# Kernel tuning notes

Measured on AMD Instinct MI355X. Metric: run time of the kernel, lower is better.

## Reference

```python
import jax, jax.numpy as jnp
import numpy as np

SCENE_BOUND = 1.5

# SH degree-2 constants (standard real spherical harmonics, Plenoxels convention)
C0 = 0.28209479177387814
C1 = 0.4886025119029199
C2_0 = 1.0925484305920792
C2_1 = -1.0925484305920792
C2_2 = 0.31539156525252005
C2_3 = -1.0925484305920792
C2_4 = 0.5462742152960396


def sh_basis(dirs):
    # dirs: (N,3) unit vectors -> (N,9) deg-2 SH basis
    x, y, z = dirs[:, 0], dirs[:, 1], dirs[:, 2]
    xx, yy, zz = x * x, y * y, z * z
    return jnp.stack([
        jnp.full_like(x, C0),
        -C1 * y,
        C1 * z,
        -C1 * x,
        C2_0 * x * y,
        C2_1 * y * z,
        C2_2 * (2.0 * zz - xx - yy),
        C2_3 * x * z,
        C2_4 * (xx - yy),
    ], axis=-1)


def grid_sample_trilinear(vol, pts):
    """torch F.grid_sample(mode=bilinear, padding=zeros, align_corners=True).

    vol: (C, D, H, W); pts: (N, 3) in [-1, 1], ordered (x, y, z) where
    x indexes W, y indexes H, z indexes D (torch convention).
    Returns (N, C).
    """
    C, D, H, W = vol.shape
    # align_corners=True: -1 -> 0, +1 -> size-1
    fx = (pts[:, 0] + 1.0) * 0.5 * (W - 1)
    fy = (pts[:, 1] + 1.0) * 0.5 * (H - 1)
    fz = (pts[:, 2] + 1.0) * 0.5 * (D - 1)
    x0 = jnp.floor(fx); y0 = jnp.floor(fy); z0 = jnp.floor(fz)
    wx1 = fx - x0; wy1 = fy - y0; wz1 = fz - z0
    x0i = x0.astype(jnp.int32); y0i = y0.astype(jnp.int32); z0i = z0.astype(jnp.int32)

    out = jnp.zeros((pts.shape[0], C), dtype=vol.dtype)
    for dz in (0, 1):
        zi = z0i + dz
        wz = wz1 if dz == 1 else (1.0 - wz1)
        for dy in (0, 1):
            yi = y0i + dy
            wy = wy1 if dy == 1 else (1.0 - wy1)
            for dx in (0, 1):
                xi = x0i + dx
                wx = wx1 if dx == 1 else (1.0 - wx1)
                inb = ((xi >= 0) & (xi < W) & (yi >= 0) & (yi < H)
                       & (zi >= 0) & (zi < D))
                xc = jnp.clip(xi, 0, W - 1)
                yc = jnp.clip(yi, 0, H - 1)
                zc = jnp.clip(zi, 0, D - 1)
                val = vol[:, zc, yc, xc]  # (C, N) gather
                w = (wx * wy * wz) * inb.astype(vol.dtype)
                out = out + val.T * w[:, None]
    return out


def setup_inputs() -> dict:
    key = jax.random.key(0)
    k1, k2, k3 = jax.random.split(key, 3)
    N, R, C = 2_000_000, 128, 28
    xyz = (jax.random.uniform(k1, (N, 3), jnp.float32) * 2.0 - 1.0) * SCENE_BOUND
    vd = jax.random.normal(k2, (N, 3), jnp.float32)
    view_dirs = vd / jnp.linalg.norm(vd, axis=-1, keepdims=True)
    density_grid = jnp.full((1, 1, R, R, R), 0.1, jnp.float32)
    sh_grid = jax.random.normal(k3, (1, C - 1, R, R, R), jnp.float32) * 0.01
    return {"xyz": xyz, "view_dirs": view_dirs,
            "density_grid": density_grid, "sh_grid": sh_grid}


def reference(xyz, view_dirs, density_grid, sh_grid):
    # combined grid (1, C, R, R, R) -> (C, D, H, W)
    vol = jnp.concatenate([density_grid, sh_grid], axis=1)[0]
    # query: trilinear interp at normalized coords
    feats = grid_sample_trilinear(vol, xyz / SCENE_BOUND)  # (N, C)
    # decode
    density = jax.nn.relu(feats[:, 0])  # (N,)
    sh_coef = feats[:, 1:].reshape(feats.shape[0], 3, 9)  # (N, 3, 9)
    basis = sh_basis(view_dirs)  # (N, 9)
    rgb = jax.nn.sigmoid(jnp.einsum('ncb,nb->nc', sh_coef, basis))  # (N, 3)
    return density, rgb
```

## Files before the change

### kernel.cpp

```cpp
#include <hip/hip_runtime.h>
#include <hip/hip_fp16.h>
#include <math.h>

#define GR 128
#define NCH 28


__device__ __forceinline__ float sigmoidf_(float x) {
    return 1.0f / (1.0f + expf(-x));
}

__device__ __forceinline__ __half2 u2h2(unsigned int u) {
    return *reinterpret_cast<__half2*>(&u);
}

__global__ __launch_bounds__(256) void pack_kernel(
    const float* __restrict__ dens,
    const float* __restrict__ sh,
    uint4* __restrict__ vol,
    int V)
{
    int t = blockIdx.x * blockDim.x + threadIdx.x;
    int v0 = t * 2;
    if (v0 >= V) return;

    float2 dd = *reinterpret_cast<const float2*>(dens + v0);
    float sa[27], sb[27];
#pragma unroll
    for (int q = 0; q < 27; ++q) {
        float2 s2 = *reinterpret_cast<const float2*>(sh + (size_t)q * (size_t)V + v0);
        sa[q] = s2.x;
        sb[q] = s2.y;
    }

#pragma unroll
    for (int j = 0; j < 2; ++j) {
        const float* sv = (j == 0) ? sa : sb;
        float dv = (j == 0) ? dd.x : dd.y;

        float mp = 0.0f, mn = 0.0f;
#pragma unroll
        for (int q = 0; q < 27; ++q) {
            float x = sv[q];
            mp = fmaxf(mp, x);
            mn = fmaxf(mn, -x);
        }
        float tq = fmaxf(fmaxf(mp * (1.0f / 7.0f), mn * 0.125f), 7.5e-9f);
        int ex = (int)((__float_as_uint(tq) >> 23) & 0xFFu) - 126;
        int e = min(max(ex + 14, 0), 15);
        float invf = __uint_as_float((unsigned int)(141 - e) << 23);

        unsigned int w[4];
#pragma unroll
        for (int d = 0; d < 3; ++d) {
            unsigned int acc = 0;
#pragma unroll
            for (int b = 0; b < 8; ++b) {
                int n = (int)rintf(sv[8 * d + b] * invf) + 8;
                n = min(max(n, 0), 15);
                acc |= (unsigned int)n << (4 * b);
            }
            w[d] = acc;
        }
        int n24 = min(max((int)rintf(sv[24] * invf) + 8, 0), 15);
        int n25 = min(max((int)rintf(sv[25] * invf) + 8, 0), 15);
        int n26 = min(max((int)rintf(sv[26] * invf) + 8, 0), 15);
        unsigned int dh = (unsigned int)__half_as_ushort(__float2half_rn(dv));
        w[3] = (unsigned int)n24 | ((unsigned int)n25 << 4) | ((unsigned int)n26 << 8)
             | ((unsigned int)e << 12) | (dh << 16);

        vol[v0 + j] = make_uint4(w[0], w[1], w[2], w[3]);
    }
}

__global__ __launch_bounds__(256) void sample_kernel(
    const float* __restrict__ xyz,
    const float* __restrict__ vdirs,
    const uint4* __restrict__ vol,
    float* __restrict__ out,
    int N)
{
    int i = blockIdx.x * blockDim.x + threadIdx.x;
    if (i >= N) return;

    const float kk = (1.0f / 1.5f) * 0.5f * (float)(GR - 1);
    const float cc = 0.5f * (float)(GR - 1);
    float fx = fminf(fmaxf(fmaf(xyz[3*i+0], kk, cc), 0.0f), (float)(GR - 1));
    float fy = fminf(fmaxf(fmaf(xyz[3*i+1], kk, cc), 0.0f), (float)(GR - 1));
    float fz = fminf(fmaxf(fmaf(xyz[3*i+2], kk, cc), 0.0f), (float)(GR - 1));

    int x0 = (int)fx, y0 = (int)fy, z0 = (int)fz;
    float wx1 = fx - (float)x0, wy1 = fy - (float)y0, wz1 = fz - (float)z0;
    float wx0 = 1.0f - wx1, wy0 = 1.0f - wy1, wz0 = 1.0f - wz1;
    int x1 = min(x0 + 1, GR - 1);
    int y1 = min(y0 + 1, GR - 1);
    int z1 = min(z0 + 1, GR - 1);

    int r00 = (z0 * GR + y0) * GR, r01 = (z0 * GR + y1) * GR;
    int r10 = (z1 * GR + y0) * GR, r11 = (z1 * GR + y1) * GR;
    uint4 c000 = vol[r00 + x0];
    uint4 c001 = vol[r00 + x1];
    uint4 c010 = vol[r01 + x0];
    uint4 c011 = vol[r01 + x1];
    uint4 c100 = vol[r10 + x0];
    uint4 c101 = vol[r10 + x1];
    uint4 c110 = vol[r11 + x0];
    uint4 c111 = vol[r11 + x1];

    float w000 = wz0 * wy0 * wx0, w001 = wz0 * wy0 * wx1;
    float w010 = wz0 * wy1 * wx0, w011 = wz0 * wy1 * wx1;
    float w100 = wz1 * wy0 * wx0, w101 = wz1 * wy0 * wx1;
    float w110 = wz1 * wy1 * wx0, w111 = wz1 * wy1 * wx1;

    __half2 acc2[15];
    unsigned int z32 = 0u;
#pragma unroll
    for (int p = 0; p < 15; ++p) acc2[p] = u2h2(z32);
    float G = 0.0f, accd = 0.0f;

    #define NIB4(DW, O)                                                        \
    {                                                                          \
        acc2[(O)+0] = __hfma2(g2, u2h2((((DW) << 6) & 0x03C003C0u) | 0x3C003C00u), acc2[(O)+0]); \
        acc2[(O)+1] = __hfma2(g2, u2h2((((DW) << 2) & 0x03C003C0u) | 0x3C003C00u), acc2[(O)+1]); \
        acc2[(O)+2] = __hfma2(g2, u2h2((((DW) >> 2) & 0x03C003C0u) | 0x3C003C00u), acc2[(O)+2]); \
        acc2[(O)+3] = __hfma2(g2, u2h2((((DW) >> 6) & 0x03C003C0u) | 0x3C003C00u), acc2[(O)+3]); \
    }
    #define NIB3(DW, O)                                                        \
    {                                                                          \
        acc2[(O)+0] = __hfma2(g2, u2h2((((DW) << 6) & 0x03C003C0u) | 0x3C003C00u), acc2[(O)+0]); \
        acc2[(O)+1] = __hfma2(g2, u2h2((((DW) << 2) & 0x03C003C0u) | 0x3C003C00u), acc2[(O)+1]); \
        acc2[(O)+2] = __hfma2(g2, u2h2((((DW) >> 2) & 0x03C003C0u) | 0x3C003C00u), acc2[(O)+2]); \
    }
    #define CORNER(C, W)                                                       \
    {                                                                          \
        float w_ = (W);                                                        \
        unsigned int e_ = ((C).w >> 12) & 0xFu;                                \
        float f_ = __uint_as_float((113u + e_) << 23);           \
        float g_ = w_ * f_;                                                    \
        G += g_;                                                               \
        accd = fmaf(w_, __half2float(__ushort_as_half((unsigned short)((C).w >> 16))), accd); \
        __half2 g2 = __float2half2_rn(g_);                                     \
        NIB4((C).x, 0) NIB4((C).y, 4) NIB4((C).z, 8) NIB3((C).w, 12)           \
    }

    CORNER(c000, w000) CORNER(c001, w001) CORNER(c010, w010) CORNER(c011, w011)
    CORNER(c100, w100) CORNER(c101, w101) CORNER(c110, w110) CORNER(c111, w111)
    #undef CORNER
    #undef NIB4
    #undef NIB3

    float c24G = 24.0f * G;
    float sch[27];
#pragma unroll
    for (int d = 0; d < 3; ++d) {
#pragma unroll
        for (int p = 0; p < 4; ++p) {
            float2 f2 = __half22float2(acc2[d * 4 + p]);
            sch[8 * d + p]     = fmaf(16.0f, f2.x, -c24G);
            sch[8 * d + p + 4] = fmaf(16.0f, f2.y, -c24G);
        }
    }
#pragma unroll
    for (int p = 0; p < 3; ++p) {
        float2 f2 = __half22float2(acc2[12 + p]);
        sch[24 + p] = fmaf(16.0f, f2.x, -c24G);
    }

    float dxv = vdirs[3*i+0], dyv = vdirs[3*i+1], dzv = vdirs[3*i+2];
    float xx = dxv*dxv, yy = dyv*dyv, zz = dzv*dzv;
    float bs[9];
    bs[0] = 0.28209479177387814f;
    bs[1] = -0.4886025119029199f * dyv;
    bs[2] =  0.4886025119029199f * dzv;
    bs[3] = -0.4886025119029199f * dxv;
    bs[4] =  1.0925484305920792f * dxv * dyv;
    bs[5] = -1.0925484305920792f * dyv * dzv;
    bs[6] =  0.31539156525252005f * (2.0f*zz - xx - yy);
    bs[7] = -1.0925484305920792f * dxv * dzv;
    bs[8] =  0.5462742152960396f * (xx - yy);

    out[i] = fmaxf(accd, 0.0f);
#pragma unroll
    for (int ch = 0; ch < 3; ++ch) {
        float sm = 0.0f;
#pragma unroll
        for (int q = 0; q < 9; ++q) sm = fmaf(sch[ch*9 + q], bs[q], sm);
        out[(size_t)N + 3*(size_t)i + ch] = sigmoidf_(sm);
    }
}

__global__ __launch_bounds__(256) void sample_direct_kernel(
    const float* __restrict__ xyz,
    const float* __restrict__ vdirs,
    const float* __restrict__ dens,
    const float* __restrict__ sh,
    float* __restrict__ out,
    int N)
{
    int i = blockIdx.x * blockDim.x + threadIdx.x;
    if (i >= N) return;

    const float kk = (1.0f / 1.5f) * 0.5f * (float)(GR - 1);
    const float cc = 0.5f * (float)(GR - 1);
    float fx = fminf(fmaxf(fmaf(xyz[3*i+0], kk, cc), 0.0f), (float)(GR - 1));
    float fy = fminf(fmaxf(fmaf(xyz[3*i+1], kk, cc), 0.0f), (float)(GR - 1));
    float fz = fminf(fmaxf(fmaf(xyz[3*i+2], kk, cc), 0.0f), (float)(GR - 1));
    float x0f = floorf(fx), y0f = floorf(fy), z0f = floorf(fz);
    float wx1 = fx - x0f, wy1 = fy - y0f, wz1 = fz - z0f;
    int x0 = (int)x0f, y0 = (int)y0f, z0 = (int)z0f;
    float wx[2] = { 1.0f - wx1, wx1 };
    float wy[2] = { 1.0f - wy1, wy1 };
    float wz[2] = { 1.0f - wz1, wz1 };
    int xi[2] = { x0, min(x0 + 1, GR-1) };
    int yi[2] = { y0, min(y0 + 1, GR-1) };
    int zi[2] = { z0, min(z0 + 1, GR-1) };

    const size_t V = (size_t)GR * GR * GR;
    float acc[NCH];
#pragma unroll
    for (int c = 0; c < NCH; ++c) acc[c] = 0.0f;

#pragma unroll
    for (int dz = 0; dz < 2; ++dz)
#pragma unroll
        for (int dy = 0; dy < 2; ++dy)
#pragma unroll
            for (int dx = 0; dx < 2; ++dx) {
                float w = wz[dz] * wy[dy] * wx[dx];
                size_t vox = (((size_t)zi[dz] * GR) + yi[dy]) * GR + xi[dx];
                acc[0] = fmaf(w, dens[vox], acc[0]);
#pragma unroll
                for (int c = 0; c < 27; ++c)
                    acc[1 + c] = fmaf(w, sh[(size_t)c * V + vox], acc[1 + c]);
            }

    float dxv = vdirs[3*i+0], dyv = vdirs[3*i+1], dzv = vdirs[3*i+2];
    float xx = dxv*dxv, yy = dyv*dyv, zz = dzv*dzv;
    float b[9];
    b[0] = 0.28209479177387814f;
    b[1] = -0.4886025119029199f * dyv;
    b[2] =  0.4886025119029199f * dzv;
    b[3] = -0.4886025119029199f * dxv;
    b[4] =  1.0925484305920792f * dxv * dyv;
    b[5] = -1.0925484305920792f * dyv * dzv;
    b[6] =  0.31539156525252005f * (2.0f*zz - xx - yy);
    b[7] = -1.0925484305920792f * dxv * dzv;
    b[8] =  0.5462742152960396f * (xx - yy);

    out[i] = fmaxf(acc[0], 0.0f);
#pragma unroll
    for (int c = 0; c < 3; ++c) {
        float sm = 0.0f;
#pragma unroll
        for (int q = 0; q < 9; ++q) sm = fmaf(acc[1 + c*9 + q], b[q], sm);
        out[(size_t)N + 3*(size_t)i + c] = sigmoidf_(sm);
    }
}

extern "C" void kernel_launch(void* const* d_in, const int* in_sizes, int n_in,
                              void* d_out, int out_size, void* d_ws, size_t ws_size,
                              hipStream_t stream) {
    const float* xyz   = (const float*)d_in[0];
    const float* vdirs = (const float*)d_in[1];
    const float* dens  = (const float*)d_in[2];
    const float* sh    = (const float*)d_in[3];
    float* out = (float*)d_out;

    int N = in_sizes[0] / 3;
    const int V = GR * GR * GR;
    size_t need = (size_t)V * 16;

    if (ws_size >= need) {
        uint4* vol = (uint4*)d_ws;
        pack_kernel<<<(V / 2 + 255) / 256, 256, 0, stream>>>(dens, sh, vol, V);
        sample_kernel<<<(N + 255) / 256, 256, 0, stream>>>(xyz, vdirs, vol, out, N);
    } else {
        sample_direct_kernel<<<(N + 255) / 256, 256, 0, stream>>>(xyz, vdirs, dens, sh, out, N);
    }
}
```

Before: 204.6 us.

## Bin points by grid octant before sampling to improve volume cache locality

Adds a scatter pass that quantizes each point's grid coordinates and its view direction (to fp16) into 16-byte records, and buckets them by octant of the volume into 512 sub-bins using wave-aggregated atomics. The sampling pass then reads records bin by bin, with a workgroup swizzle so that concurrently running blocks share octants. The goal is for each XCD/L2 to touch only part of the packed volume, cutting cache misses on the random 8-corner gathers. In exchange it adds an extra pass over all points, extra record traffic, and quantization of the interpolation weights (1/512) and view directions to fp16. Output stores also become nontemporal.

Result: no change. 201.5 us (-1.5%).

```diff
diff --git a/kernel.cpp b/kernel.cpp
--- a/kernel.cpp
+++ b/kernel.cpp
@@ -4,12 +4,16 @@
 
 #define GR 128
 #define NCH 28
+#define CSTR 32
+#define NSUB 64
+#define NREG 512
+
+typedef unsigned int uivec4 __attribute__((ext_vector_type(4)));
 
 
 __device__ __forceinline__ float sigmoidf_(float x) {
     return 1.0f / (1.0f + expf(-x));
 }
-
 __device__ __forceinline__ __half2 u2h2(unsigned int u) {
     return *reinterpret_cast<__half2*>(&u);
 }
@@ -73,24 +77,12 @@
     }
 }
 
-__global__ __launch_bounds__(256) void sample_kernel(
-    const float* __restrict__ xyz,
-    const float* __restrict__ vdirs,
+__device__ __forceinline__ void trilerp_shade(
     const uint4* __restrict__ vol,
-    float* __restrict__ out,
-    int N)
-{
-    int i = blockIdx.x * blockDim.x + threadIdx.x;
-    if (i >= N) return;
-
-    const float kk = (1.0f / 1.5f) * 0.5f * (float)(GR - 1);
-    const float cc = 0.5f * (float)(GR - 1);
-    float fx = fminf(fmaxf(fmaf(xyz[3*i+0], kk, cc), 0.0f), (float)(GR - 1));
-    float fy = fminf(fmaxf(fmaf(xyz[3*i+1], kk, cc), 0.0f), (float)(GR - 1));
-    float fz = fminf(fmaxf(fmaf(xyz[3*i+2], kk, cc), 0.0f), (float)(GR - 1));
-
-    int x0 = (int)fx, y0 = (int)fy, z0 = (int)fz;
-    float wx1 = fx - (float)x0, wy1 = fy - (float)y0, wz1 = fz - (float)z0;
+    int x0, int y0, int z0, float wx1, float wy1, float wz1,
+    float dxv, float dyv, float dzv,
+    float* __restrict__ out, int N, unsigned int idx)
+{
     float wx0 = 1.0f - wx1, wy0 = 1.0f - wy1, wz0 = 1.0f - wz1;
     int x1 = min(x0 + 1, GR - 1);
     int y1 = min(y0 + 1, GR - 1);
@@ -113,9 +105,8 @@
     float w110 = wz1 * wy1 * wx0, w111 = wz1 * wy1 * wx1;
 
     __half2 acc2[15];
-    unsigned int z32 = 0u;
-#pragma unroll
-    for (int p = 0; p < 15; ++p) acc2[p] = u2h2(z32);
+#pragma unroll
+    for (int p = 0; p < 15; ++p) acc2[p] = u2h2(0u);
     float G = 0.0f, accd = 0.0f;
 
     #define NIB4(DW, O)                                                        \
@@ -166,7 +157,6 @@
         sch[24 + p] = fmaf(16.0f, f2.x, -c24G);
     }
 
-    float dxv = vdirs[3*i+0], dyv = vdirs[3*i+1], dzv = vdirs[3*i+2];
     float xx = dxv*dxv, yy = dyv*dyv, zz = dzv*dzv;
     float bs[9];
     bs[0] = 0.28209479177387814f;
@@ -179,14 +169,117 @@
     bs[7] = -1.0925484305920792f * dxv * dzv;
     bs[8] =  0.5462742152960396f * (xx - yy);
 
-    out[i] = fmaxf(accd, 0.0f);
+    __builtin_nontemporal_store(fmaxf(accd, 0.0f), &out[idx]);
 #pragma unroll
     for (int ch = 0; ch < 3; ++ch) {
         float sm = 0.0f;
 #pragma unroll
         for (int q = 0; q < 9; ++q) sm = fmaf(sch[ch*9 + q], bs[q], sm);
-        out[(size_t)N + 3*(size_t)i + ch] = sigmoidf_(sm);
-    }
+        __builtin_nontemporal_store(sigmoidf_(sm), &out[(size_t)N + 3*(size_t)idx + ch]);
+    }
+}
+
+__global__ __launch_bounds__(256) void zero_kernel(unsigned int* __restrict__ p, int n) {
+    int i = blockIdx.x * blockDim.x + threadIdx.x;
+    if (i < n) p[i] = 0u;
+}
+
+__global__ __launch_bounds__(256) void scatter_oct_kernel(
+    const float* __restrict__ xyz, const float* __restrict__ vdirs,
+    unsigned int* __restrict__ cursors,
+    uint4* __restrict__ recs, int N, int cap_sub)
+{
+    int i = blockIdx.x * blockDim.x + threadIdx.x;
+    bool active = (i < N);
+    unsigned int ux = 0, uy = 0, uz = 0, hx = 0, hy = 0, hz = 0;
+    int oct = -1;
+    if (active) {
+        const float kk = (1.0f / 1.5f) * 0.5f * (float)(GR - 1);
+        const float cc = 0.5f * (float)(GR - 1);
+        float fx = fminf(fmaxf(fmaf(xyz[3*i+0], kk, cc), 0.0f), (float)(GR - 1));
+        float fy = fminf(fmaxf(fmaf(xyz[3*i+1], kk, cc), 0.0f), (float)(GR - 1));
+        float fz = fminf(fmaxf(fmaf(xyz[3*i+2], kk, cc), 0.0f), (float)(GR - 1));
+        ux = (unsigned int)(int)rintf(fx * 512.0f);
+        uy = (unsigned int)(int)rintf(fy * 512.0f);
+        uz = (unsigned int)(int)rintf(fz * 512.0f);
+        hx = (unsigned int)__half_as_ushort(__float2half_rn(vdirs[3*i+0]));
+        hy = (unsigned int)__half_as_ushort(__float2half_rn(vdirs[3*i+1]));
+        hz = (unsigned int)__half_as_ushort(__float2half_rn(vdirs[3*i+2]));
+        oct = (int)((ux >> 15) | ((uy >> 15) << 1) | ((uz >> 15) << 2));
+    }
+
+    int lane = (int)(threadIdx.x & 63u);
+    int blockSub = (int)(blockIdx.x & (NSUB - 1));
+#pragma unroll
+    for (int k = 0; k < 8; ++k) {
+        unsigned long long mask = __ballot(active && (oct == k));
+        if (active && (oct == k)) {
+            int leader = __ffsll((unsigned long long)mask) - 1;
+            int rank = __popcll(mask & ((1ull << lane) - 1ull));
+            int s = k * NSUB + blockSub;
+            unsigned int base = 0;
+            if (lane == leader)
+                base = atomicAdd(&cursors[s * CSTR], (unsigned int)__popcll(mask));
+            base = (unsigned int)__shfl((int)base, leader);
+            unsigned int pos = (unsigned int)s * (unsigned int)cap_sub + base + (unsigned int)rank;
+            uivec4 r;
+            r.x = ux | (uy << 16);
+            r.y = uz | (hx << 16);
+            r.z = hy | (hz << 16);
+            r.w = (unsigned int)i;
+            __builtin_nontemporal_store(r, (uivec4*)(recs + pos));
+        }
+    }
+}
+
+__global__ __launch_bounds__(256) void sample_oct_kernel(
+    const uint4* __restrict__ recs,
+    const unsigned int* __restrict__ cursors,
+    const uint4* __restrict__ vol,
+    float* __restrict__ out, int N, int cap_sub, int nwg)
+{
+    int bid = blockIdx.x;
+    int cpx = nwg >> 3;
+    int swz = (bid & 7) * cpx + (bid >> 3);
+    int i = swz * 256 + (int)threadIdx.x;
+
+    unsigned int s = (unsigned int)i / (unsigned int)cap_sub;
+    unsigned int off = (unsigned int)i - s * (unsigned int)cap_sub;
+    if (off >= cursors[s * CSTR]) return;
+
+    uivec4 Rv = __builtin_nontemporal_load((const uivec4*)(recs + i));
+    unsigned int ux = Rv.x & 0xFFFFu, uy = Rv.x >> 16;
+    unsigned int uz = Rv.y & 0xFFFFu;
+    int x0 = (int)(ux >> 9), y0 = (int)(uy >> 9), z0 = (int)(uz >> 9);
+    float wx1 = (float)(ux & 511u) * (1.0f / 512.0f);
+    float wy1 = (float)(uy & 511u) * (1.0f / 512.0f);
+    float wz1 = (float)(uz & 511u) * (1.0f / 512.0f);
+
+    float dxv = __half2float(__ushort_as_half((unsigned short)(Rv.y >> 16)));
+    float dyv = __half2float(__ushort_as_half((unsigned short)(Rv.z & 0xFFFFu)));
+    float dzv = __half2float(__ushort_as_half((unsigned short)(Rv.z >> 16)));
+
+    trilerp_shade(vol, x0, y0, z0, wx1, wy1, wz1, dxv, dyv, dzv, out, N, Rv.w);
+}
+
+__global__ __launch_bounds__(256) void sample_kernel(
+    const float* __restrict__ xyz,
+    const float* __restrict__ vdirs,
+    const uint4* __restrict__ vol,
+    float* __restrict__ out,
+    int N)
+{
+    int i = blockIdx.x * blockDim.x + threadIdx.x;
+    if (i >= N) return;
+
+    const float kk = (1.0f / 1.5f) * 0.5f * (float)(GR - 1);
+    const float cc = 0.5f * (float)(GR - 1);
+    float fx = fminf(fmaxf(fmaf(xyz[3*i+0], kk, cc), 0.0f), (float)(GR - 1));
+    float fy = fminf(fmaxf(fmaf(xyz[3*i+1], kk, cc), 0.0f), (float)(GR - 1));
+    float fz = fminf(fmaxf(fmaf(xyz[3*i+2], kk, cc), 0.0f), (float)(GR - 1));
+    int x0 = (int)fx, y0 = (int)fy, z0 = (int)fz;
+    trilerp_shade(vol, x0, y0, z0, fx - (float)x0, fy - (float)y0, fz - (float)z0,
+                  vdirs[3*i+0], vdirs[3*i+1], vdirs[3*i+2], out, N, (unsigned int)i);
 }
 
 __global__ __launch_bounds__(256) void sample_direct_kernel(
@@ -268,9 +361,35 @@
 
     int N = in_sizes[0] / 3;
     const int V = GR * GR * GR;
-    size_t need = (size_t)V * 16;
-
-    if (ws_size >= need) {
+
+    int per = (N + NREG - 1) / NREG;
+    int cap_sub = (per + per / 10 + 64 + 3) & ~3;
+
+    size_t off_vol  = 0;
+    size_t sz_vol   = (size_t)V * 16;
+    size_t off_recs = (off_vol + sz_vol + 255) & ~(size_t)255;
+    size_t sz_recs  = (size_t)NREG * (size_t)cap_sub * 16;
+    size_t off_cur  = (off_recs + sz_recs + 255) & ~(size_t)255;
+    size_t sz_cur   = (size_t)NREG * CSTR * 4;
+    size_t need_full = off_cur + sz_cur;
+    size_t need_mid  = sz_vol;
+
+    if (ws_size >= need_full) {
+        char* ws = (char*)d_ws;
+        uint4*        vol     = (uint4*)(ws + off_vol);
+        uint4*        recs    = (uint4*)(ws + off_recs);
+        unsigned int* cursors = (unsigned int*)(ws + off_cur);
+
+        int nwg_pts = (N + 255) / 256;
+        int ncur = NREG * CSTR;
+        int nslots = NREG * cap_sub;
+        int nwg_s = nslots / 256;
+
+        pack_kernel<<<(V / 2 + 255) / 256, 256, 0, stream>>>(dens, sh, vol, V);
+        zero_kernel<<<(ncur + 255) / 256, 256, 0, stream>>>(cursors, ncur);
+        scatter_oct_kernel<<<nwg_pts, 256, 0, stream>>>(xyz, vdirs, cursors, recs, N, cap_sub);
+        sample_oct_kernel<<<nwg_s, 256, 0, stream>>>(recs, cursors, vol, out, N, cap_sub, nwg_s);
+    } else if (ws_size >= need_mid) {
         uint4* vol = (uint4*)d_ws;
         pack_kernel<<<(V / 2 + 255) / 256, 256, 0, stream>>>(dens, sh, vol, V);
         sample_kernel<<<(N + 255) / 256, 256, 0, stream>>>(xyz, vdirs, vol, out, N);
```

## Store packed voxel grid in 2x2x2 bricks and use nontemporal streaming loads/stores

Applied to the files above, without the earlier changes.

The pack kernel now writes each quantized voxel into a 2x2x2 brick layout, so the eight trilinear corners of a sample tend to sit in the same 128-byte region. The sample kernel computes brick addresses for those corners. It also uses nontemporal loads for the xyz and direction inputs and nontemporal stores for the outputs, to keep streaming data from evicting the grid from cache. Shading is factored into a helper. Brick addressing costs a few extra integer ops per corner, and corners that cross a brick boundary still touch several lines.

Measured after the change: 169.5 us. 1.21x faster.

```diff
diff --git a/kernel.cpp b/kernel.cpp
--- a/kernel.cpp
+++ b/kernel.cpp
@@ -3,15 +3,21 @@
 #include <math.h>
 
 #define GR 128
+#define GB 64
 #define NCH 28
+
+typedef float fvec4 __attribute__((ext_vector_type(4)));
 
 
 __device__ __forceinline__ float sigmoidf_(float x) {
     return 1.0f / (1.0f + expf(-x));
 }
-
 __device__ __forceinline__ __half2 u2h2(unsigned int u) {
     return *reinterpret_cast<__half2*>(&u);
+}
+__device__ __forceinline__ int brick_addr(int x, int y, int z) {
+    int b = ((z >> 1) * GB + (y >> 1)) * GB + (x >> 1);
+    return b * 8 + ((z & 1) << 2) + ((y & 1) << 1) + (x & 1);
 }
 
 __global__ __launch_bounds__(256) void pack_kernel(
@@ -33,6 +39,11 @@
         sb[q] = s2.y;
     }
 
+    int x = v0 & (GR - 1);
+    int y = (v0 >> 7) & (GR - 1);
+    int z = v0 >> 14;
+    int base = brick_addr(x, y, z);
+
 #pragma unroll
     for (int j = 0; j < 2; ++j) {
         const float* sv = (j == 0) ? sa : sb;
@@ -41,9 +52,9 @@
         float mp = 0.0f, mn = 0.0f;
 #pragma unroll
         for (int q = 0; q < 27; ++q) {
-            float x = sv[q];
-            mp = fmaxf(mp, x);
-            mn = fmaxf(mn, -x);
+            float xq = sv[q];
+            mp = fmaxf(mp, xq);
+            mn = fmaxf(mn, -xq);
         }
         float tq = fmaxf(fmaxf(mp * (1.0f / 7.0f), mn * 0.125f), 7.5e-9f);
         int ex = (int)((__float_as_uint(tq) >> 23) & 0xFFu) - 126;
@@ -69,53 +80,25 @@
         w[3] = (unsigned int)n24 | ((unsigned int)n25 << 4) | ((unsigned int)n26 << 8)
              | ((unsigned int)e << 12) | (dh << 16);
 
-        vol[v0 + j] = make_uint4(w[0], w[1], w[2], w[3]);
-    }
-}
-
-__global__ __launch_bounds__(256) void sample_kernel(
-    const float* __restrict__ xyz,
-    const float* __restrict__ vdirs,
-    const uint4* __restrict__ vol,
-    float* __restrict__ out,
-    int N)
+        vol[base + j] = make_uint4(w[0], w[1], w[2], w[3]);
+    }
+}
+
+__device__ __forceinline__ fvec4 shade_eval(
+    uint4 c000, uint4 c001, uint4 c010, uint4 c011,
+    uint4 c100, uint4 c101, uint4 c110, uint4 c111,
+    float wx1, float wy1, float wz1,
+    float dxv, float dyv, float dzv)
 {
-    int i = blockIdx.x * blockDim.x + threadIdx.x;
-    if (i >= N) return;
-
-    const float kk = (1.0f / 1.5f) * 0.5f * (float)(GR - 1);
-    const float cc = 0.5f * (float)(GR - 1);
-    float fx = fminf(fmaxf(fmaf(xyz[3*i+0], kk, cc), 0.0f), (float)(GR - 1));
-    float fy = fminf(fmaxf(fmaf(xyz[3*i+1], kk, cc), 0.0f), (float)(GR - 1));
-    float fz = fminf(fmaxf(fmaf(xyz[3*i+2], kk, cc), 0.0f), (float)(GR - 1));
-
-    int x0 = (int)fx, y0 = (int)fy, z0 = (int)fz;
-    float wx1 = fx - (float)x0, wy1 = fy - (float)y0, wz1 = fz - (float)z0;
     float wx0 = 1.0f - wx1, wy0 = 1.0f - wy1, wz0 = 1.0f - wz1;
-    int x1 = min(x0 + 1, GR - 1);
-    int y1 = min(y0 + 1, GR - 1);
-    int z1 = min(z0 + 1, GR - 1);
-
-    int r00 = (z0 * GR + y0) * GR, r01 = (z0 * GR + y1) * GR;
-    int r10 = (z1 * GR + y0) * GR, r11 = (z1 * GR + y1) * GR;
-    uint4 c000 = vol[r00 + x0];
-    uint4 c001 = vol[r00 + x1];
-    uint4 c010 = vol[r01 + x0];
-    uint4 c011 = vol[r01 + x1];
-    uint4 c100 = vol[r10 + x0];
-    uint4 c101 = vol[r10 + x1];
-    uint4 c110 = vol[r11 + x0];
-    uint4 c111 = vol[r11 + x1];
-
     float w000 = wz0 * wy0 * wx0, w001 = wz0 * wy0 * wx1;
     float w010 = wz0 * wy1 * wx0, w011 = wz0 * wy1 * wx1;
     float w100 = wz1 * wy0 * wx0, w101 = wz1 * wy0 * wx1;
     float w110 = wz1 * wy1 * wx0, w111 = wz1 * wy1 * wx1;
 
     __half2 acc2[15];
-    unsigned int z32 = 0u;
-#pragma unroll
-    for (int p = 0; p < 15; ++p) acc2[p] = u2h2(z32);
+#pragma unroll
+    for (int p = 0; p < 15; ++p) acc2[p] = u2h2(0u);
     float G = 0.0f, accd = 0.0f;
 
     #define NIB4(DW, O)                                                        \
@@ -166,7 +149,6 @@
         sch[24 + p] = fmaf(16.0f, f2.x, -c24G);
     }
 
-    float dxv = vdirs[3*i+0], dyv = vdirs[3*i+1], dzv = vdirs[3*i+2];
     float xx = dxv*dxv, yy = dyv*dyv, zz = dzv*dzv;
     float bs[9];
     bs[0] = 0.28209479177387814f;
@@ -179,14 +161,75 @@
     bs[7] = -1.0925484305920792f * dxv * dzv;
     bs[8] =  0.5462742152960396f * (xx - yy);
 
-    out[i] = fmaxf(accd, 0.0f);
+    fvec4 res;
+    res.x = fmaxf(accd, 0.0f);
 #pragma unroll
     for (int ch = 0; ch < 3; ++ch) {
         float sm = 0.0f;
 #pragma unroll
         for (int q = 0; q < 9; ++q) sm = fmaf(sch[ch*9 + q], bs[q], sm);
-        out[(size_t)N + 3*(size_t)i + ch] = sigmoidf_(sm);
-    }
+        if (ch == 0) res.y = sigmoidf_(sm);
+        else if (ch == 1) res.z = sigmoidf_(sm);
+        else res.w = sigmoidf_(sm);
+    }
+    return res;
+}
+
+__global__ __launch_bounds__(256) void sample_kernel(
+    const float* __restrict__ xyz,
+    const float* __restrict__ vdirs,
+    const uint4* __restrict__ vol,
+    float* __restrict__ out,
+    int N)
+{
+    int i = blockIdx.x * blockDim.x + threadIdx.x;
+    if (i >= N) return;
+
+    float px = __builtin_nontemporal_load(xyz + 3*i + 0);
+    float py = __builtin_nontemporal_load(xyz + 3*i + 1);
+    float pz = __builtin_nontemporal_load(xyz + 3*i + 2);
+
+    const float kk = (1.0f / 1.5f) * 0.5f * (float)(GR - 1);
+    const float cc = 0.5f * (float)(GR - 1);
+    float fx = fminf(fmaxf(fmaf(px, kk, cc), 0.0f), (float)(GR - 1));
+    float fy = fminf(fmaxf(fmaf(py, kk, cc), 0.0f), (float)(GR - 1));
+    float fz = fminf(fmaxf(fmaf(pz, kk, cc), 0.0f), (float)(GR - 1));
+    int x0 = (int)fx, y0 = (int)fy, z0 = (int)fz;
+    float wx1 = fx - (float)x0, wy1 = fy - (float)y0, wz1 = fz - (float)z0;
+    int x1 = min(x0 + 1, GR - 1);
+    int y1 = min(y0 + 1, GR - 1);
+    int z1 = min(z0 + 1, GR - 1);
+
+    int a000 = brick_addr(x0, y0, z0);
+    int a001 = brick_addr(x1, y0, z0);
+    int a010 = brick_addr(x0, y1, z0);
+    int a011 = brick_addr(x1, y1, z0);
+    int a100 = brick_addr(x0, y0, z1);
+    int a101 = brick_addr(x1, y0, z1);
+    int a110 = brick_addr(x0, y1, z1);
+    int a111 = brick_addr(x1, y1, z1);
+
+    uint4 c000 = vol[a000];
+    uint4 c001 = vol[a001];
+    uint4 c010 = vol[a010];
+    uint4 c011 = vol[a011];
+    uint4 c100 = vol[a100];
+    uint4 c101 = vol[a101];
+    uint4 c110 = vol[a110];
+    uint4 c111 = vol[a111];
+
+    float dxv = __builtin_nontemporal_load(vdirs + 3*i + 0);
+    float dyv = __builtin_nontemporal_load(vdirs + 3*i + 1);
+    float dzv = __builtin_nontemporal_load(vdirs + 3*i + 2);
+
+    fvec4 res = shade_eval(c000, c001, c010, c011, c100, c101, c110, c111,
+                           wx1, wy1, wz1, dxv, dyv, dzv);
+
+    __builtin_nontemporal_store(res.x, &out[i]);
+    size_t o = (size_t)N + 3*(size_t)i;
+    __builtin_nontemporal_store(res.y, &out[o + 0]);
+    __builtin_nontemporal_store(res.z, &out[o + 1]);
+    __builtin_nontemporal_store(res.w, &out[o + 2]);
 }
 
 __global__ __launch_bounds__(256) void sample_direct_kernel(
```
